# Kernel tuning notes

Hardware: AMD Instinct MI355X
Metric: run time of the kernel (lower is better)

Reference implementation:

```python
import jax, jax.numpy as jnp
import numpy as np

# Config matching init_kwargs
B, C, H, W = 16, 256, 128, 128
RED, MID, NHEADS, G, WS = 64, 32, 4, 4, 8
SCALE = (MID // NHEADS) ** -0.5
EPS = 1e-5


def _bn(x, gamma, beta, mean, var):
    # eval-mode BatchNorm2d over channel dim of NCHW
    inv = gamma / jnp.sqrt(var + EPS)
    return x * inv[None, :, None, None] + (beta - mean * inv)[None, :, None, None]


def _gconv1d(x, w, b=None):
    # grouped 1x1 Conv1d: x (B, Cin, N), w (G, Cout_g, Cin_g)
    Bx, Cin, N = x.shape
    g, cout_g, cin_g = w.shape
    xg = x.reshape(Bx, g, cin_g, N)
    y = jnp.einsum('bgin,goi->bgon', xg, w).reshape(Bx, g * cout_g, N)
    if b is not None:
        y = y + b[None, :, None]
    return y


def setup_inputs() -> dict:
    key = jax.random.key(0)
    ks = jax.random.split(key, 20)
    s = 0.05
    d = {
        'x': jax.random.normal(ks[0], (B, C, H, W), jnp.float32),
        'bn_in_gamma': jnp.ones((C,), jnp.float32),
        'bn_in_beta': jnp.zeros((C,), jnp.float32),
        'bn_in_mean': jax.random.normal(ks[1], (C,), jnp.float32) * s,
        'bn_in_var': jax.random.uniform(ks[2], (C,), jnp.float32, 0.5, 1.5),
        'in_proj_w': jax.random.normal(ks[3], (RED, C), jnp.float32) * s,
        'qk_base_w': jax.random.normal(ks[4], (G, MID // G, RED // G), jnp.float32) * s,
        'q_head_w': jax.random.normal(ks[5], (MID, MID), jnp.float32) * s,
        'q_head_b': jnp.zeros((MID,), jnp.float32),
        'k_head_w': jax.random.normal(ks[6], (MID, MID), jnp.float32) * s,
        'k_head_b': jnp.zeros((MID,), jnp.float32),
        'v_w': jax.random.normal(ks[7], (G, MID // G, RED // G), jnp.float32) * s,
        'v_b': jnp.zeros((MID,), jnp.float32),
        'o_w': jax.random.normal(ks[8], (G, RED // G, MID // G), jnp.float32) * s,
        'o_b': jnp.zeros((RED,), jnp.float32),
        'out_proj_w': jax.random.normal(ks[9], (C, RED), jnp.float32) * s,
        'bn_out_gamma': jnp.ones((C,), jnp.float32),
        'bn_out_beta': jnp.zeros((C,), jnp.float32),
        'bn_out_mean': jax.random.normal(ks[10], (C,), jnp.float32) * s,
        'bn_out_var': jax.random.uniform(ks[11], (C,), jnp.float32, 0.5, 1.5),
        'alpha': jnp.zeros((), jnp.float32),
    }
    return d


def reference(x, bn_in_gamma, bn_in_beta, bn_in_mean, bn_in_var, in_proj_w,
              qk_base_w, q_head_w, q_head_b, k_head_w, k_head_b,
              v_w, v_b, o_w, o_b, out_proj_w,
              bn_out_gamma, bn_out_beta, bn_out_mean, bn_out_var, alpha):
    identity = x
    xn = _bn(x, bn_in_gamma, bn_in_beta, bn_in_mean, bn_in_var)
    x_red = jnp.einsum('oc,bchw->bohw', in_proj_w, xn)  # (B, RED, H, W)

    # window partition (H, W divisible by WS -> no padding)
    nH, nW = H // WS, W // WS
    xw = x_red.reshape(B, RED, nH, WS, nW, WS)
    xw = xw.transpose(0, 2, 4, 1, 3, 5).reshape(B * nH * nW, RED, WS * WS)

    # attention on N = WS*WS tokens per window
    base = _gconv1d(xw, qk_base_w)                              # (Bw, MID, N)
    q = jnp.einsum('oi,bin->bon', q_head_w, base) + q_head_b[None, :, None]
    k = jnp.einsum('oi,bin->bon', k_head_w, base) + k_head_b[None, :, None]
    v = _gconv1d(xw, v_w, v_b)

    def split_heads(t):
        Bw, Cm, N = t.shape
        return t.reshape(Bw, NHEADS, Cm // NHEADS, N).transpose(0, 1, 3, 2)  # (Bw,h,N,hd)

    q, k, v = split_heads(q), split_heads(k), split_heads(v)
    attn = jax.nn.softmax(jnp.einsum('bhnd,bhmd->bhnm', q, k) * SCALE, axis=-1)
    out = jnp.einsum('bhnm,bhmd->bhnd', attn, v)                # (Bw,h,N,hd)
    Bw = out.shape[0]
    out = out.transpose(0, 1, 3, 2).reshape(Bw, MID, WS * WS)
    out = _gconv1d(out, o_w, o_b)                               # (Bw, RED, N)

    # merge windows
    out = out.reshape(B, nH, nW, RED, WS, WS)
    out = out.transpose(0, 3, 1, 4, 2, 5).reshape(B, RED, H, W)

    out = jnp.einsum('oc,bchw->bohw', out_proj_w, out)          # (B, C, H, W)
    out = _bn(out, bn_out_gamma, bn_out_beta, bn_out_mean, bn_out_var)
    return identity + jax.nn.sigmoid(alpha) * out
```

## Files before the change

### kernel.cpp

```cpp
#include <hip/hip_runtime.h>
#include <math.h>

constexpr int Bb   = 16;
constexpr int Cc   = 256;
constexpr int Hh   = 128;
constexpr int Ww   = 128;
constexpr int NPIX = Hh * Ww;
constexpr int RED  = 64;
constexpr int MID  = 32;
constexpr float SCALE = 0.35355339059327373f;

__global__ __launch_bounds__(256) void prep_kernel(
    const float* __restrict__ bn_in_gamma, const float* __restrict__ bn_in_beta,
    const float* __restrict__ bn_in_mean,  const float* __restrict__ bn_in_var,
    const float* __restrict__ in_proj_w,
    const float* __restrict__ out_proj_w,
    const float* __restrict__ bn_out_gamma, const float* __restrict__ bn_out_beta,
    const float* __restrict__ bn_out_mean,  const float* __restrict__ bn_out_var,
    const float* __restrict__ alpha,
    float* __restrict__ Weff_in,  float* __restrict__ beff_in,
    float* __restrict__ Weff_out, float* __restrict__ beff_out) {
  int idx = blockIdx.x * 256 + threadIdx.x;
  float s = 1.0f / (1.0f + __expf(-alpha[0]));
  if (idx < RED * Cc) {
    int c = idx & 255;
    float inv = bn_in_gamma[c] * rsqrtf(bn_in_var[c] + 1e-5f);
    Weff_in[idx] = in_proj_w[idx] * inv;
  }
  if (idx < Cc * RED) {
    int co = idx >> 6;
    float inv2 = bn_out_gamma[co] * rsqrtf(bn_out_var[co] + 1e-5f);
    Weff_out[idx] = s * inv2 * out_proj_w[idx];
  }
  if (idx < RED) {
    float acc = 0.f;
    for (int c = 0; c < Cc; c++) {
      float inv = bn_in_gamma[c] * rsqrtf(bn_in_var[c] + 1e-5f);
      acc += in_proj_w[idx * Cc + c] * (bn_in_beta[c] - bn_in_mean[c] * inv);
    }
    beff_in[idx] = acc;
  }
  if (idx < Cc) {
    float inv2 = bn_out_gamma[idx] * rsqrtf(bn_out_var[idx] + 1e-5f);
    beff_out[idx] = s * (bn_out_beta[idx] - bn_out_mean[idx] * inv2);
  }
}

__global__ __launch_bounds__(256) void inproj_kernel(
    const float* __restrict__ x, const float* __restrict__ Weff,
    const float* __restrict__ beff, float* __restrict__ xred) {
  __shared__ float Xs[32][128];
  __shared__ float Ws[32][64];
  const int b  = blockIdx.y;
  const int p0 = blockIdx.x * 128;
  const int tid = threadIdx.x;
  const int tx = tid & 31;
  const int ty = tid >> 5;
  const int o0 = ty * 8;

  float acc[8][4];
  #pragma unroll
  for (int i = 0; i < 8; i++) {
    float bia = beff[o0 + i];
    #pragma unroll
    for (int j = 0; j < 4; j++) acc[i][j] = bia;
  }

  const float* xb = x + ((size_t)b * Cc) * NPIX + p0;
  for (int c0 = 0; c0 < Cc; c0 += 32) {
    __syncthreads();
    for (int f = tid; f < 1024; f += 256) {
      int c = f >> 5, pq = f & 31;
      ((float4*)Xs[c])[pq] = *(const float4*)(xb + (size_t)(c0 + c) * NPIX + pq * 4);
    }
    for (int e = tid; e < 2048; e += 256) {
      int o = e & 63, ci = e >> 6;
      Ws[ci][o] = Weff[o * Cc + c0 + ci];
    }
    __syncthreads();
    #pragma unroll
    for (int c = 0; c < 32; c++) {
      float4 xv = ((const float4*)Xs[c])[tx];
      float4 w0 = ((const float4*)Ws[c])[ty * 2];
      float4 w1 = ((const float4*)Ws[c])[ty * 2 + 1];
      float xa[4] = {xv.x, xv.y, xv.z, xv.w};
      float wa[8] = {w0.x, w0.y, w0.z, w0.w, w1.x, w1.y, w1.z, w1.w};
      #pragma unroll
      for (int i = 0; i < 8; i++)
        #pragma unroll
        for (int j = 0; j < 4; j++) acc[i][j] += wa[i] * xa[j];
    }
  }
  float* op = xred + ((size_t)b * RED) * NPIX + p0 + tx * 4;
  #pragma unroll
  for (int i = 0; i < 8; i++) {
    *(float4*)(op + (size_t)(o0 + i) * NPIX) =
        make_float4(acc[i][0], acc[i][1], acc[i][2], acc[i][3]);
  }
}

__global__ __launch_bounds__(256) void attn_kernel(
    const float* __restrict__ xred,
    const float* __restrict__ qk_base_w, const float* __restrict__ q_head_w,
    const float* __restrict__ q_head_b,  const float* __restrict__ k_head_w,
    const float* __restrict__ k_head_b,  const float* __restrict__ v_w,
    const float* __restrict__ v_b,       const float* __restrict__ o_w,
    const float* __restrict__ o_b,       float* __restrict__ yout) {
  __shared__ float smem[13952];
  float* Xw    = smem;
  float* base_ = smem + 4096;
  float* kT    = smem + 6144;
  float* vT    = smem + 8256;
  float* qkw   = smem + 10368;
  float* vw    = smem + 10880;
  float* ow    = smem + 11392;
  float* qhw   = smem + 11904;
  float* khw   = smem + 12928;
  float* outT  = smem;

  const int w  = blockIdx.x;
  const int b  = w >> 8;
  const int wh = (w >> 4) & 15, wwi = w & 15;
  const int tid = threadIdx.x;
  const float* xb = xred + ((size_t)b * RED) * NPIX + (wh * 8) * Ww + wwi * 8;

  for (int e = tid; e < 4096; e += 256) {
    int r = e >> 6, n = e & 63;
    Xw[e] = xb[(size_t)r * NPIX + (n >> 3) * Ww + (n & 7)];
  }
  for (int e = tid; e < 512; e += 256) { qkw[e] = qk_base_w[e]; vw[e] = v_w[e]; ow[e] = o_w[e]; }
  for (int e = tid; e < 1024; e += 256) { qhw[e] = q_head_w[e]; khw[e] = k_head_w[e]; }
  __syncthreads();

  for (int e = tid; e < 2048; e += 256) {
    int m = e >> 6, n = e & 63, g = m >> 3;
    const float* wp = qkw + (g * 8 + (m & 7)) * 16;
    const float* xp = Xw + g * 16 * 64 + n;
    float a = 0.f;
    #pragma unroll
    for (int i = 0; i < 16; i++) a += wp[i] * xp[i * 64];
    base_[e] = a;
  }
  __syncthreads();

  for (int e = tid; e < 2048; e += 256) {
    int m = e >> 6, n = e & 63, g = m >> 3;
    float a = k_head_b[m];
    const float* wp = khw + m * 32;
    #pragma unroll
    for (int i = 0; i < 32; i++) a += wp[i] * base_[i * 64 + n];
    kT[n * 33 + m] = a;
    float av = v_b[m];
    const float* vp = vw + (g * 8 + (m & 7)) * 16;
    const float* xp = Xw + g * 16 * 64 + n;
    #pragma unroll
    for (int i = 0; i < 16; i++) av += vp[i] * xp[i * 64];
    vT[n * 33 + m] = av;
  }
  __syncthreads();

  const int h = tid >> 6, n = tid & 63;
  float qv[8];
  {
    float a[8];
    #pragma unroll
    for (int d = 0; d < 8; d++) a[d] = q_head_b[h * 8 + d];
    #pragma unroll
    for (int i = 0; i < 32; i++) {
      float bv = base_[i * 64 + n];
      #pragma unroll
      for (int d = 0; d < 8; d++) a[d] += qhw[(h * 8 + d) * 32 + i] * bv;
    }
    #pragma unroll
    for (int d = 0; d < 8; d++) qv[d] = a[d] * SCALE;
  }
  float s[64];
  float mx = -1e30f;
  const float* kTh = kT + h * 8;
  #pragma unroll
  for (int j = 0; j < 64; j++) {
    const float* kr = kTh + j * 33;
    float a = 0.f;
    #pragma unroll
    for (int d = 0; d < 8; d++) a += qv[d] * kr[d];
    s[j] = a;
    mx = fmaxf(mx, a);
  }
  float sum = 0.f;
  #pragma unroll
  for (int j = 0; j < 64; j++) { float e = __expf(s[j] - mx); s[j] = e; sum += e; }
  float inv = 1.0f / sum;
  float o[8] = {0, 0, 0, 0, 0, 0, 0, 0};
  const float* vTh = vT + h * 8;
  #pragma unroll
  for (int j = 0; j < 64; j++) {
    float p = s[j];
    const float* vr = vTh + j * 33;
    #pragma unroll
    for (int d = 0; d < 8; d++) o[d] += p * vr[d];
  }
  __syncthreads();
  #pragma unroll
  for (int d = 0; d < 8; d++) outT[n * 33 + h * 8 + d] = o[d] * inv;
  __syncthreads();

  float* yb = yout + ((size_t)b * RED) * NPIX + (wh * 8) * Ww + wwi * 8;
  for (int e = tid; e < 4096; e += 256) {
    int r = e >> 6, nn = e & 63, g = r >> 4;
    float a = o_b[r];
    const float* wp = ow + (g * 16 + (r & 15)) * 8;
    const float* op = outT + nn * 33 + g * 8;
    #pragma unroll
    for (int j = 0; j < 8; j++) a += wp[j] * op[j];
    yb[(size_t)r * NPIX + (nn >> 3) * Ww + (nn & 7)] = a;
  }
}

__global__ __launch_bounds__(256) void outproj_kernel(
    const float* __restrict__ y, const float* __restrict__ Weff,
    const float* __restrict__ beff, const float* __restrict__ x,
    float* __restrict__ out) {
  __shared__ float Ys[64][128];
  __shared__ float Ws[64][64];
  const int b   = blockIdx.z;
  const int co0 = blockIdx.y * 64;
  const int p0  = blockIdx.x * 128;
  const int tid = threadIdx.x;
  const int tx = tid & 31, ty = tid >> 5;
  const int ol = ty * 8;

  const float* yb = y + ((size_t)b * RED) * NPIX + p0;
  for (int f = tid; f < 2048; f += 256) {
    int r = f >> 5, pq = f & 31;
    ((float4*)Ys[r])[pq] = *(const float4*)(yb + (size_t)r * NPIX + pq * 4);
  }
  for (int e = tid; e < 4096; e += 256) {
    int co = e & 63, r = e >> 6;
    Ws[r][co] = Weff[(size_t)(co0 + co) * RED + r];
  }
  __syncthreads();

  float acc[8][4];
  #pragma unroll
  for (int i = 0; i < 8; i++) {
    float bia = beff[co0 + ol + i];
    #pragma unroll
    for (int j = 0; j < 4; j++) acc[i][j] = bia;
  }
  #pragma unroll
  for (int r = 0; r < 64; r++) {
    float4 xv = ((const float4*)Ys[r])[tx];
    float4 w0 = ((const float4*)Ws[r])[ty * 2];
    float4 w1 = ((const float4*)Ws[r])[ty * 2 + 1];
    float xa[4] = {xv.x, xv.y, xv.z, xv.w};
    float wa[8] = {w0.x, w0.y, w0.z, w0.w, w1.x, w1.y, w1.z, w1.w};
    #pragma unroll
    for (int i = 0; i < 8; i++)
      #pragma unroll
      for (int j = 0; j < 4; j++) acc[i][j] += wa[i] * xa[j];
  }

  const float* xb = x + ((size_t)b * Cc + co0) * NPIX + p0 + tx * 4;
  float* ob = out + ((size_t)b * Cc + co0) * NPIX + p0 + tx * 4;
  #pragma unroll
  for (int i = 0; i < 8; i++) {
    float4 xv = *(const float4*)(xb + (size_t)(ol + i) * NPIX);
    *(float4*)(ob + (size_t)(ol + i) * NPIX) =
        make_float4(acc[i][0] + xv.x, acc[i][1] + xv.y,
                    acc[i][2] + xv.z, acc[i][3] + xv.w);
  }
}

extern "C" void kernel_launch(void* const* d_in, const int* in_sizes, int n_in,
                              void* d_out, int out_size, void* d_ws, size_t ws_size,
                              hipStream_t stream) {
  const float* x           = (const float*)d_in[0];
  const float* bn_in_gamma = (const float*)d_in[1];
  const float* bn_in_beta  = (const float*)d_in[2];
  const float* bn_in_mean  = (const float*)d_in[3];
  const float* bn_in_var   = (const float*)d_in[4];
  const float* in_proj_w   = (const float*)d_in[5];
  const float* qk_base_w   = (const float*)d_in[6];
  const float* q_head_w    = (const float*)d_in[7];
  const float* q_head_b    = (const float*)d_in[8];
  const float* k_head_w    = (const float*)d_in[9];
  const float* k_head_b    = (const float*)d_in[10];
  const float* v_w         = (const float*)d_in[11];
  const float* v_b         = (const float*)d_in[12];
  const float* o_w         = (const float*)d_in[13];
  const float* o_b         = (const float*)d_in[14];
  const float* out_proj_w  = (const float*)d_in[15];
  const float* bn_out_gamma= (const float*)d_in[16];
  const float* bn_out_beta = (const float*)d_in[17];
  const float* bn_out_mean = (const float*)d_in[18];
  const float* bn_out_var  = (const float*)d_in[19];
  const float* alpha       = (const float*)d_in[20];

  float* ws = (float*)d_ws;
  float* Weff_in  = ws;
  float* beff_in  = Weff_in + 16384;
  float* Weff_out = beff_in + 64;
  float* beff_out = Weff_out + 16384;
  float* xred     = beff_out + 256;
  float* ybuf     = xred + (size_t)16777216;
  (void)ws_size; (void)in_sizes; (void)n_in; (void)out_size;

  prep_kernel<<<64, 256, 0, stream>>>(
      bn_in_gamma, bn_in_beta, bn_in_mean, bn_in_var, in_proj_w,
      out_proj_w, bn_out_gamma, bn_out_beta, bn_out_mean, bn_out_var,
      alpha, Weff_in, beff_in, Weff_out, beff_out);

  inproj_kernel<<<dim3(128, 16), 256, 0, stream>>>(x, Weff_in, beff_in, xred);

  attn_kernel<<<4096, 256, 0, stream>>>(
      xred, qk_base_w, q_head_w, q_head_b, k_head_w, k_head_b,
      v_w, v_b, o_w, o_b, ybuf);

  outproj_kernel<<<dim3(128, 4, 16), 256, 0, stream>>>(
      ybuf, Weff_out, beff_out, x, (float*)d_out);
}
```

Before: 890.9 us.

## Fuse in-proj, window attention and out-proj into one per-window kernel

Merges the three main kernels into a single per-window kernel, so the 64-channel reduced activations and attention outputs never round-trip through global memory. The grouped o_w projection is folded algebraically into the out-proj weights on the host-side prep kernel, shrinking the final GEMM from 64 to 32 inputs. Blocks are remapped so neighbouring windows are spread across the grid. The trade-off is uncoalesced 8-wide window loads and stores of x and out, plus weight reads straight from global/L1 inside the inner loops, with a launch_bounds occupancy hint.

```diff
diff --git a/kernel.cpp b/kernel.cpp
--- a/kernel.cpp
+++ b/kernel.cpp
@@ -17,20 +17,26 @@
     const float* __restrict__ out_proj_w,
     const float* __restrict__ bn_out_gamma, const float* __restrict__ bn_out_beta,
     const float* __restrict__ bn_out_mean,  const float* __restrict__ bn_out_var,
+    const float* __restrict__ o_w, const float* __restrict__ o_b,
     const float* __restrict__ alpha,
-    float* __restrict__ Weff_in,  float* __restrict__ beff_in,
-    float* __restrict__ Weff_out, float* __restrict__ beff_out) {
+    float* __restrict__ WtIn,  float* __restrict__ beff_in,
+    float* __restrict__ WtCmb, float* __restrict__ bcomb) {
   int idx = blockIdx.x * 256 + threadIdx.x;
   float s = 1.0f / (1.0f + __expf(-alpha[0]));
-  if (idx < RED * Cc) {
-    int c = idx & 255;
+  if (idx < Cc * RED) {
+    int c = idx >> 6, r = idx & 63;
     float inv = bn_in_gamma[c] * rsqrtf(bn_in_var[c] + 1e-5f);
-    Weff_in[idx] = in_proj_w[idx] * inv;
-  }
-  if (idx < Cc * RED) {
-    int co = idx >> 6;
+    WtIn[idx] = in_proj_w[r * Cc + c] * inv;
+  }
+  if (idx < MID * Cc) {
+    int m = idx >> 8, co = idx & 255;
+    int g = m >> 3, j = m & 7;
     float inv2 = bn_out_gamma[co] * rsqrtf(bn_out_var[co] + 1e-5f);
-    Weff_out[idx] = s * inv2 * out_proj_w[idx];
+    float a = 0.f;
+    #pragma unroll
+    for (int t = 0; t < 16; t++)
+      a += out_proj_w[co * RED + g * 16 + t] * o_w[g * 128 + t * 8 + j];
+    WtCmb[idx] = s * inv2 * a;
   }
   if (idx < RED) {
     float acc = 0.f;
@@ -42,100 +48,77 @@
   }
   if (idx < Cc) {
     float inv2 = bn_out_gamma[idx] * rsqrtf(bn_out_var[idx] + 1e-5f);
-    beff_out[idx] = s * (bn_out_beta[idx] - bn_out_mean[idx] * inv2);
+    float a = bn_out_beta[idx] - bn_out_mean[idx] * inv2;
+    for (int r = 0; r < RED; r++)
+      a += inv2 * out_proj_w[idx * RED + r] * o_b[r];
+    bcomb[idx] = s * a;
   }
 }
 
-__global__ __launch_bounds__(256) void inproj_kernel(
-    const float* __restrict__ x, const float* __restrict__ Weff,
-    const float* __restrict__ beff, float* __restrict__ xred) {
-  __shared__ float Xs[32][128];
-  __shared__ float Ws[32][64];
-  const int b  = blockIdx.y;
-  const int p0 = blockIdx.x * 128;
-  const int tid = threadIdx.x;
-  const int tx = tid & 31;
-  const int ty = tid >> 5;
-  const int o0 = ty * 8;
-
-  float acc[8][4];
-  #pragma unroll
-  for (int i = 0; i < 8; i++) {
-    float bia = beff[o0 + i];
-    #pragma unroll
-    for (int j = 0; j < 4; j++) acc[i][j] = bia;
-  }
-
-  const float* xb = x + ((size_t)b * Cc) * NPIX + p0;
-  for (int c0 = 0; c0 < Cc; c0 += 32) {
-    __syncthreads();
-    for (int f = tid; f < 1024; f += 256) {
-      int c = f >> 5, pq = f & 31;
-      ((float4*)Xs[c])[pq] = *(const float4*)(xb + (size_t)(c0 + c) * NPIX + pq * 4);
-    }
-    for (int e = tid; e < 2048; e += 256) {
-      int o = e & 63, ci = e >> 6;
-      Ws[ci][o] = Weff[o * Cc + c0 + ci];
-    }
-    __syncthreads();
-    #pragma unroll
-    for (int c = 0; c < 32; c++) {
-      float4 xv = ((const float4*)Xs[c])[tx];
-      float4 w0 = ((const float4*)Ws[c])[ty * 2];
-      float4 w1 = ((const float4*)Ws[c])[ty * 2 + 1];
-      float xa[4] = {xv.x, xv.y, xv.z, xv.w};
-      float wa[8] = {w0.x, w0.y, w0.z, w0.w, w1.x, w1.y, w1.z, w1.w};
-      #pragma unroll
-      for (int i = 0; i < 8; i++)
-        #pragma unroll
-        for (int j = 0; j < 4; j++) acc[i][j] += wa[i] * xa[j];
-    }
-  }
-  float* op = xred + ((size_t)b * RED) * NPIX + p0 + tx * 4;
-  #pragma unroll
-  for (int i = 0; i < 8; i++) {
-    *(float4*)(op + (size_t)(o0 + i) * NPIX) =
-        make_float4(acc[i][0], acc[i][1], acc[i][2], acc[i][3]);
-  }
-}
-
-__global__ __launch_bounds__(256) void attn_kernel(
-    const float* __restrict__ xred,
+__global__ __launch_bounds__(256, 3) void fused_kernel(
+    const float* __restrict__ x,
+    const float* __restrict__ WtIn,
+    const float* __restrict__ beff_in,
     const float* __restrict__ qk_base_w, const float* __restrict__ q_head_w,
     const float* __restrict__ q_head_b,  const float* __restrict__ k_head_w,
     const float* __restrict__ k_head_b,  const float* __restrict__ v_w,
-    const float* __restrict__ v_b,       const float* __restrict__ o_w,
-    const float* __restrict__ o_b,       float* __restrict__ yout) {
-  __shared__ float smem[13952];
-  float* Xw    = smem;
+    const float* __restrict__ v_b,
+    const float* __restrict__ WtCmb,
+    const float* __restrict__ bcomb,
+    float* __restrict__ out) {
+  __shared__ float smem[13440];
+  float* XR    = smem;
   float* base_ = smem + 4096;
   float* kT    = smem + 6144;
   float* vT    = smem + 8256;
   float* qkw   = smem + 10368;
   float* vw    = smem + 10880;
-  float* ow    = smem + 11392;
-  float* qhw   = smem + 11904;
-  float* khw   = smem + 12928;
-  float* outT  = smem;
-
-  const int w  = blockIdx.x;
-  const int b  = w >> 8;
-  const int wh = (w >> 4) & 15, wwi = w & 15;
-  const int tid = threadIdx.x;
-  const float* xb = xred + ((size_t)b * RED) * NPIX + (wh * 8) * Ww + wwi * 8;
-
-  for (int e = tid; e < 4096; e += 256) {
-    int r = e >> 6, n = e & 63;
-    Xw[e] = xb[(size_t)r * NPIX + (n >> 3) * Ww + (n & 7)];
-  }
-  for (int e = tid; e < 512; e += 256) { qkw[e] = qk_base_w[e]; vw[e] = v_w[e]; ow[e] = o_w[e]; }
+  float* qhw   = smem + 11392;
+  float* khw   = smem + 12416;
+  float* Xc    = smem + 4096;
+  float* outT  = base_;
+
+  const int bid = blockIdx.x;
+  const int w   = ((bid & 7) << 9) | (bid >> 3);
+  const int b   = w >> 8;
+  const int wh  = (w >> 4) & 15, wwi = w & 15;
+  const int tid  = threadIdx.x;
+  const int lane = tid & 63;
+  const int wv   = __builtin_amdgcn_readfirstlane(tid >> 6);
+
+  const float* xwin = x + ((size_t)b * Cc) * NPIX + (wh * 8) * Ww + wwi * 8;
+
+  float acc[16];
+  #pragma unroll
+  for (int t = 0; t < 16; t++) acc[t] = beff_in[wv * 16 + t];
+  for (int ch = 0; ch < 4; ch++) {
+    __syncthreads();
+    for (int e = tid; e < 1024; e += 256) {
+      int cc = e >> 4, nq = e & 15;
+      int i = nq >> 1, half = nq & 1;
+      float4 xv4 = *(const float4*)(xwin + (size_t)(ch * 64 + cc) * NPIX + i * Ww + half * 4);
+      *(float4*)(Xc + cc * 64 + nq * 4) = xv4;
+    }
+    __syncthreads();
+    const float* Wp = WtIn + (size_t)(ch * 64) * 64 + wv * 16;
+    #pragma unroll
+    for (int k = 0; k < 64; k++) {
+      float xv = Xc[k * 64 + lane];
+      const float* wk = Wp + k * 64;
+      #pragma unroll
+      for (int t = 0; t < 16; t++) acc[t] = fmaf(wk[t], xv, acc[t]);
+    }
+  }
+  #pragma unroll
+  for (int t = 0; t < 16; t++) XR[(wv * 16 + t) * 64 + lane] = acc[t];
+  for (int e = tid; e < 512; e += 256)  { qkw[e] = qk_base_w[e]; vw[e] = v_w[e]; }
   for (int e = tid; e < 1024; e += 256) { qhw[e] = q_head_w[e]; khw[e] = k_head_w[e]; }
   __syncthreads();
 
   for (int e = tid; e < 2048; e += 256) {
     int m = e >> 6, n = e & 63, g = m >> 3;
     const float* wp = qkw + (g * 8 + (m & 7)) * 16;
-    const float* xp = Xw + g * 16 * 64 + n;
+    const float* xp = XR + g * 16 * 64 + n;
     float a = 0.f;
     #pragma unroll
     for (int i = 0; i < 16; i++) a += wp[i] * xp[i * 64];
@@ -152,31 +135,30 @@
     kT[n * 33 + m] = a;
     float av = v_b[m];
     const float* vp = vw + (g * 8 + (m & 7)) * 16;
-    const float* xp = Xw + g * 16 * 64 + n;
+    const float* xp = XR + g * 16 * 64 + n;
     #pragma unroll
     for (int i = 0; i < 16; i++) av += vp[i] * xp[i * 64];
     vT[n * 33 + m] = av;
   }
   __syncthreads();
 
-  const int h = tid >> 6, n = tid & 63;
   float qv[8];
   {
     float a[8];
     #pragma unroll
-    for (int d = 0; d < 8; d++) a[d] = q_head_b[h * 8 + d];
+    for (int d = 0; d < 8; d++) a[d] = q_head_b[wv * 8 + d];
     #pragma unroll
     for (int i = 0; i < 32; i++) {
-      float bv = base_[i * 64 + n];
+      float bv = base_[i * 64 + lane];
       #pragma unroll
-      for (int d = 0; d < 8; d++) a[d] += qhw[(h * 8 + d) * 32 + i] * bv;
+      for (int d = 0; d < 8; d++) a[d] += qhw[(wv * 8 + d) * 32 + i] * bv;
     }
     #pragma unroll
     for (int d = 0; d < 8; d++) qv[d] = a[d] * SCALE;
   }
   float s[64];
   float mx = -1e30f;
-  const float* kTh = kT + h * 8;
+  const float* kTh = kT + wv * 8;
   #pragma unroll
   for (int j = 0; j < 64; j++) {
     const float* kr = kTh + j * 33;
@@ -191,7 +173,7 @@
   for (int j = 0; j < 64; j++) { float e = __expf(s[j] - mx); s[j] = e; sum += e; }
   float inv = 1.0f / sum;
   float o[8] = {0, 0, 0, 0, 0, 0, 0, 0};
-  const float* vTh = vT + h * 8;
+  const float* vTh = vT + wv * 8;
   #pragma unroll
   for (int j = 0; j < 64; j++) {
     float p = s[j];
@@ -201,73 +183,30 @@
   }
   __syncthreads();
   #pragma unroll
-  for (int d = 0; d < 8; d++) outT[n * 33 + h * 8 + d] = o[d] * inv;
-  __syncthreads();
-
-  float* yb = yout + ((size_t)b * RED) * NPIX + (wh * 8) * Ww + wwi * 8;
-  for (int e = tid; e < 4096; e += 256) {
-    int r = e >> 6, nn = e & 63, g = r >> 4;
-    float a = o_b[r];
-    const float* wp = ow + (g * 16 + (r & 15)) * 8;
-    const float* op = outT + nn * 33 + g * 8;
-    #pragma unroll
-    for (int j = 0; j < 8; j++) a += wp[j] * op[j];
-    yb[(size_t)r * NPIX + (nn >> 3) * Ww + (nn & 7)] = a;
-  }
-}
-
-__global__ __launch_bounds__(256) void outproj_kernel(
-    const float* __restrict__ y, const float* __restrict__ Weff,
-    const float* __restrict__ beff, const float* __restrict__ x,
-    float* __restrict__ out) {
-  __shared__ float Ys[64][128];
-  __shared__ float Ws[64][64];
-  const int b   = blockIdx.z;
-  const int co0 = blockIdx.y * 64;
-  const int p0  = blockIdx.x * 128;
-  const int tid = threadIdx.x;
-  const int tx = tid & 31, ty = tid >> 5;
-  const int ol = ty * 8;
-
-  const float* yb = y + ((size_t)b * RED) * NPIX + p0;
-  for (int f = tid; f < 2048; f += 256) {
-    int r = f >> 5, pq = f & 31;
-    ((float4*)Ys[r])[pq] = *(const float4*)(yb + (size_t)r * NPIX + pq * 4);
-  }
-  for (int e = tid; e < 4096; e += 256) {
-    int co = e & 63, r = e >> 6;
-    Ws[r][co] = Weff[(size_t)(co0 + co) * RED + r];
-  }
-  __syncthreads();
-
-  float acc[8][4];
-  #pragma unroll
-  for (int i = 0; i < 8; i++) {
-    float bia = beff[co0 + ol + i];
-    #pragma unroll
-    for (int j = 0; j < 4; j++) acc[i][j] = bia;
-  }
-  #pragma unroll
-  for (int r = 0; r < 64; r++) {
-    float4 xv = ((const float4*)Ys[r])[tx];
-    float4 w0 = ((const float4*)Ws[r])[ty * 2];
-    float4 w1 = ((const float4*)Ws[r])[ty * 2 + 1];
-    float xa[4] = {xv.x, xv.y, xv.z, xv.w};
-    float wa[8] = {w0.x, w0.y, w0.z, w0.w, w1.x, w1.y, w1.z, w1.w};
-    #pragma unroll
-    for (int i = 0; i < 8; i++)
+  for (int d = 0; d < 8; d++) outT[(wv * 8 + d) * 64 + lane] = o[d] * inv;
+  __syncthreads();
+
+  const int ii = lane >> 3, jj = lane & 7;
+  const size_t pixoff = (size_t)(wh * 8 + ii) * Ww + wwi * 8 + jj;
+  for (int cc = 0; cc < 4; cc++) {
+    const int co0 = cc * 64 + wv * 16;
+    float oacc[16];
+    #pragma unroll
+    for (int t = 0; t < 16; t++) oacc[t] = bcomb[co0 + t];
+    const float* Wp = WtCmb + co0;
+    #pragma unroll
+    for (int k = 0; k < 32; k++) {
+      float yv = outT[k * 64 + lane];
+      const float* wk = Wp + k * 256;
       #pragma unroll
-      for (int j = 0; j < 4; j++) acc[i][j] += wa[i] * xa[j];
-  }
-
-  const float* xb = x + ((size_t)b * Cc + co0) * NPIX + p0 + tx * 4;
-  float* ob = out + ((size_t)b * Cc + co0) * NPIX + p0 + tx * 4;
-  #pragma unroll
-  for (int i = 0; i < 8; i++) {
-    float4 xv = *(const float4*)(xb + (size_t)(ol + i) * NPIX);
-    *(float4*)(ob + (size_t)(ol + i) * NPIX) =
-        make_float4(acc[i][0] + xv.x, acc[i][1] + xv.y,
-                    acc[i][2] + xv.z, acc[i][3] + xv.w);
+      for (int t = 0; t < 16; t++) oacc[t] = fmaf(wk[t], yv, oacc[t]);
+    }
+    const float* xr = x   + ((size_t)b * Cc + co0) * NPIX + pixoff;
+    float*       orr = out + ((size_t)b * Cc + co0) * NPIX + pixoff;
+    #pragma unroll
+    for (int t = 0; t < 16; t++) {
+      orr[(size_t)t * NPIX] = oacc[t] + xr[(size_t)t * NPIX];
+    }
   }
 }
 
@@ -297,25 +236,18 @@
   const float* alpha       = (const float*)d_in[20];
 
   float* ws = (float*)d_ws;
-  float* Weff_in  = ws;
-  float* beff_in  = Weff_in + 16384;
-  float* Weff_out = beff_in + 64;
-  float* beff_out = Weff_out + 16384;
-  float* xred     = beff_out + 256;
-  float* ybuf     = xred + (size_t)16777216;
+  float* WtIn    = ws;
+  float* beff_in = ws + 16384;
+  float* WtCmb   = ws + 16448;
+  float* bcomb   = ws + 24640;
   (void)ws_size; (void)in_sizes; (void)n_in; (void)out_size;
 
   prep_kernel<<<64, 256, 0, stream>>>(
       bn_in_gamma, bn_in_beta, bn_in_mean, bn_in_var, in_proj_w,
       out_proj_w, bn_out_gamma, bn_out_beta, bn_out_mean, bn_out_var,
-      alpha, Weff_in, beff_in, Weff_out, beff_out);
-
-  inproj_kernel<<<dim3(128, 16), 256, 0, stream>>>(x, Weff_in, beff_in, xred);
-
-  attn_kernel<<<4096, 256, 0, stream>>>(
-      xred, qk_base_w, q_head_w, q_head_b, k_head_w, k_head_b,
-      v_w, v_b, o_w, o_b, ybuf);
-
-  outproj_kernel<<<dim3(128, 4, 16), 256, 0, stream>>>(
-      ybuf, Weff_out, beff_out, x, (float*)d_out);
+      o_w, o_b, alpha, WtIn, beff_in, WtCmb, bcomb);
+
+  fused_kernel<<<4096, 256, 0, stream>>>(
+      x, WtIn, beff_in, qk_base_w, q_head_w, q_head_b, k_head_w, k_head_b,
+      v_w, v_b, WtCmb, bcomb, (float*)d_out);
 }
```

Result: faster. 777.7 us (-12.7%).
